# Optimization experiments

Hardware: AMD Instinct MI355X
Metric: run time of the kernel (lower is better)

Reference implementation:

```python
import jax, jax.numpy as jnp
import numpy as np

N, E = 10000, 640000
IN_FT, OUT_FT = 512, 128
NEG_SLOPE = 0.2


def setup_inputs() -> dict:
    key = jax.random.key(0)
    ks = jax.random.split(key, 10)
    seq = jax.random.normal(ks[0], (N, IN_FT), dtype=jnp.float32)
    # edges with no self-loops: dst = (src + offset) % N, offset in [1, N-1]
    src = jax.random.randint(ks[1], (E,), 0, N)
    off = jax.random.randint(ks[2], (E,), 1, N)
    dst = (src + off) % N
    edge_index = jnp.stack([src, dst]).astype(jnp.int64)
    # parameters (xavier-ish scale)
    W_fc = jax.random.normal(ks[3], (OUT_FT, IN_FT), dtype=jnp.float32) * (1.0 / np.sqrt(IN_FT))
    W_gat = jax.random.normal(ks[4], (OUT_FT, OUT_FT), dtype=jnp.float32) * (1.0 / np.sqrt(OUT_FT))
    att_src = jax.random.normal(ks[5], (OUT_FT,), dtype=jnp.float32) * 0.1
    att_dst = jax.random.normal(ks[6], (OUT_FT,), dtype=jnp.float32) * 0.1
    gat_bias = jnp.zeros((OUT_FT,), dtype=jnp.float32)
    bias = jnp.zeros((OUT_FT,), dtype=jnp.float32)
    prelu_a = jnp.asarray(0.25, dtype=jnp.float32)
    return {"seq": seq, "edge_index": edge_index, "W_fc": W_fc, "W_gat": W_gat,
            "att_src": att_src, "att_dst": att_dst, "gat_bias": gat_bias,
            "bias": bias, "prelu_a": prelu_a}


def _gat_forward(seq, src, dst, W_fc, W_gat, att_src, att_dst, gat_bias, bias, prelu_a):
    n = seq.shape[0]
    x = seq @ W_fc.T                      # [N, out_ft] fc (no bias)
    h = x @ W_gat.T                       # GATConv internal linear (no bias)
    a_s = h @ att_src                     # [N] per-node src attention logits
    a_d = h @ att_dst                     # [N]
    e = a_s[src] + a_d[dst]               # [E'] per-edge raw score
    e = jnp.where(e >= 0, e, NEG_SLOPE * e)
    # segment softmax over destination node
    m = jax.ops.segment_max(e, dst, num_segments=n)
    m = jnp.where(jnp.isfinite(m), m, 0.0)
    p = jnp.exp(e - m[dst])
    denom = jax.ops.segment_sum(p, dst, num_segments=n)
    alpha = p / (denom[dst] + 1e-16)
    msgs = alpha[:, None] * h[src]        # [E', out_ft]
    out = jax.ops.segment_sum(msgs, dst, num_segments=n) + gat_bias
    out = out + bias
    return jnp.where(out >= 0, out, prelu_a * out)  # PReLU


def reference(seq, edge_index, W_fc, W_gat, att_src, att_dst, gat_bias, bias, prelu_a):
    n = seq.shape[0]
    loops = jnp.arange(n, dtype=edge_index.dtype)   # add_self_loops
    src = jnp.concatenate([edge_index[0], loops])
    dst = jnp.concatenate([edge_index[1], loops])
    return _gat_forward(seq, src, dst, W_fc, W_gat, att_src, att_dst, gat_bias, bias, prelu_a)
```

## Files before the change

### kernel.cpp

```cpp
#include <hip/hip_runtime.h>
#include <hip/hip_bf16.h>

#define IN_FT 512
#define OUT_FT 128
#define NEG_SLOPE 0.2f
#define SHIFT_C 4.0f
#define CAP8 768
#define NBMAX 1280

typedef __attribute__((ext_vector_type(8))) short short8;
typedef __attribute__((ext_vector_type(4))) short short4v;
typedef __attribute__((ext_vector_type(4))) float float4v;

__device__ inline short f2bf_s(float x) {
    __hip_bfloat16 b = __float2bfloat16(x);
    union { __hip_bfloat16 b; short s; } u;
    u.b = b;
    return u.s;
}
__device__ inline float bf2f(short s) {
    union { float f; unsigned u; } u;
    u.u = ((unsigned)(unsigned short)s) << 16;
    return u.f;
}

__global__ void k_prep(const float* __restrict__ Wg,
                       const float* __restrict__ Wf,
                       short* __restrict__ whf,
                       int* __restrict__ gcur, int nb) {
    if (blockIdx.x >= 256) {
        int i = (blockIdx.x - 256) * 256 + threadIdx.x;
        if (i < nb) gcur[i] = 0;
        return;
    }
    int idx = blockIdx.x * blockDim.x + threadIdx.x;
    int o = idx >> 9;
    int k = idx & 511;
    float s = 0.f;
#pragma unroll 8
    for (int j = 0; j < OUT_FT; ++j)
        s += Wg[o * OUT_FT + j] * Wf[j * IN_FT + k];
    int t = o >> 4, l15 = o & 15;
    int kc = k >> 5, q = (k >> 3) & 3, jj = k & 7;
    whf[(((kc * 8 + t) * 64) + q * 16 + l15) * 8 + jj] = f2bf_s(s);
}

__launch_bounds__(256)
__global__ void k_main(const float* __restrict__ seq,
                       const short8* __restrict__ whf,
                       const float* __restrict__ att_s_v,
                       const float* __restrict__ att_d_v,
                       short* __restrict__ h16,
                       float* __restrict__ a_s,
                       float* __restrict__ a_d,
                       const int* __restrict__ src,
                       const int* __restrict__ dstv,
                       int* __restrict__ gcur,
                       unsigned* __restrict__ bins,
                       int N, int E, int nb, int GB) {
    __shared__ char smem[24576];
    if (blockIdx.x >= GB) {
        int* hist  = (int*)smem;
        int* sbase = hist + NBMAX;
        int* scur  = sbase + NBMAX;
        int e0 = (blockIdx.x - GB) * 2048;
        for (int t = threadIdx.x; t < nb; t += 256) hist[t] = 0;
        __syncthreads();
        int myd[8];
#pragma unroll
        for (int k = 0; k < 8; ++k) {
            int e = e0 + k * 256 + threadIdx.x;
            myd[k] = (e < E) ? dstv[e] : -1;
            if ((unsigned)myd[k] < (unsigned)N) atomicAdd(&hist[myd[k] >> 3], 1);
            else myd[k] = -1;
        }
        __syncthreads();
        for (int t = threadIdx.x; t < nb; t += 256) {
            int c = hist[t];
            sbase[t] = c ? atomicAdd(&gcur[t], c) : 0;
            scur[t] = 0;
        }
        __syncthreads();
#pragma unroll
        for (int k = 0; k < 8; ++k) {
            if (myd[k] >= 0) {
                int e = e0 + k * 256 + threadIdx.x;
                int b = myd[k] >> 3;
                int slot = sbase[b] + atomicAdd(&scur[b], 1);
                if (slot < CAP8) {
                    int s = src[e];
                    if ((unsigned)s >= (unsigned)N) s = 0;
                    bins[(size_t)b * CAP8 + slot] = ((unsigned)s << 3) | (myd[k] & 7);
                }
            }
        }
        return;
    }
    short* As = (short*)smem;
    float4v* red = (float4v*)smem;

    int wave = threadIdx.x >> 6;
    int lane = threadIdx.x & 63;
    int l15 = lane & 15, quad = lane >> 4;
    int rows0 = blockIdx.x * 16;

#pragma unroll
    for (int i = 0; i < 8; ++i) {
        int idx = threadIdx.x + 256 * i;
        int r = idx >> 7, c4 = idx & 127;
        int row = rows0 + r;
        int rowc = row < N ? row : N - 1;
        float4 v = *(const float4*)(seq + (size_t)rowc * IN_FT + c4 * 4);
        short4v b;
        b[0] = f2bf_s(v.x); b[1] = f2bf_s(v.y); b[2] = f2bf_s(v.z); b[3] = f2bf_s(v.w);
        int kc = c4 >> 3, q = (c4 >> 1) & 3, half = c4 & 1;
        *(short4v*)(As + (((kc * 4 + q) * 16 + r) * 8 + half * 4)) = b;
    }
    __syncthreads();

    float4v acc[8];
    for (int t = 0; t < 8; ++t) acc[t] = (float4v){0.f, 0.f, 0.f, 0.f};

#pragma unroll
    for (int kk = 0; kk < 4; ++kk) {
        int kc = wave * 4 + kk;
        short8 a = *(const short8*)(As + ((kc * 4 + quad) * 16 + l15) * 8);
        const short8* bhp = whf + (size_t)kc * 512 + lane;
#pragma unroll
        for (int t = 0; t < 8; ++t) {
            short8 bh = bhp[t * 64];
            acc[t] = __builtin_amdgcn_mfma_f32_16x16x32_bf16(a, bh, acc[t], 0, 0, 0);
        }
    }
    __syncthreads();
    if (wave > 0) {
        float4v* base = red + ((wave - 1) * 8) * 64 + lane;
        for (int t = 0; t < 8; ++t) base[t * 64] = acc[t];
    }
    __syncthreads();
    if (wave != 0) return;
    for (int w2 = 0; w2 < 3; ++w2) {
        const float4v* base = red + (w2 * 8) * 64 + lane;
        for (int t = 0; t < 8; ++t) {
            float4v v = base[t * 64];
            acc[t][0] += v[0]; acc[t][1] += v[1]; acc[t][2] += v[2]; acc[t][3] += v[3];
        }
    }
    int rbase = rows0 + quad * 4;
    for (int r = 0; r < 4; ++r) {
        int rr = rbase + r;
        if (rr < N) {
            short* hr = h16 + (size_t)rr * OUT_FT;
            for (int t = 0; t < 8; ++t) hr[t * 16 + l15] = f2bf_s(acc[t][r]);
        }
    }
    float asv[8], adv[8];
    for (int t = 0; t < 8; ++t) {
        asv[t] = att_s_v[t * 16 + l15];
        adv[t] = att_d_v[t * 16 + l15];
    }
    for (int r = 0; r < 4; ++r) {
        float ps = 0.f, pd = 0.f;
        for (int t = 0; t < 8; ++t) {
            float v = acc[t][r];
            ps += v * asv[t];
            pd += v * adv[t];
        }
        for (int m = 1; m < 16; m <<= 1) {
            ps += __shfl_xor(ps, m);
            pd += __shfl_xor(pd, m);
        }
        int rr = rbase + r;
        if (l15 == 0 && rr < N) { a_s[rr] = ps; a_d[rr] = pd; }
    }
}

__launch_bounds__(256)
__global__ void k_agg(const short* __restrict__ h16, const float* __restrict__ a_s,
                      const float* __restrict__ a_d,
                      const int* __restrict__ gcur, const unsigned* __restrict__ bins,
                      const float* __restrict__ gat_bias,
                      const float* __restrict__ bias,
                      const float* __restrict__ prelu_a,
                      float* __restrict__ out, int N) {
    __shared__ int2  spair[CAP8 + 64];
    __shared__ int   hist[8], base[8], cur8[8];
    __shared__ float ads[8];
    int b = blockIdx.x;
    int d0 = b << 3;
    int nd = N - d0; if (nd > 8) nd = 8;
    int tid = threadIdx.x;

    if (tid < 8) {
        hist[tid] = 0;
        ads[tid] = (tid < nd) ? a_d[d0 + tid] : 0.f;
    }
    __syncthreads();

    int cnt = gcur[b]; if (cnt > CAP8) cnt = CAP8;
    const unsigned* binp = bins + (size_t)b * CAP8;

    for (int c = tid; c < cnt; c += 256) atomicAdd(&hist[binp[c] & 7], 1);
    __syncthreads();
    if (tid == 0) {
        int run = 0;
        for (int i = 0; i < 8; ++i) {
            base[i] = run; cur8[i] = 0;
            run += (hist[i] + 7) & ~7;
        }
    }
    __syncthreads();
    for (int c = tid; c < cnt; c += 256) {
        unsigned pk = binp[c];
        int dl = pk & 7, sv = pk >> 3;
        float ev = a_s[sv] + ads[dl];
        ev = (ev >= 0.f) ? ev : NEG_SLOPE * ev;
        float p = __expf(ev - SHIFT_C);
        int slot = base[dl] + atomicAdd(&cur8[dl], 1);
        int2 sp; sp.x = sv; sp.y = __float_as_int(p);
        spair[slot] = sp;
    }
    if (tid < 64) {
        int dl = tid >> 3, k = tid & 7;
        int n = hist[dl], np = (n + 7) & ~7;
        if (n + k < np) {
            int2 sp; sp.x = d0; sp.y = 0;
            spair[base[dl] + n + k] = sp;
        }
    }
    __syncthreads();

    int w = tid >> 6, L = tid & 63;
    float b0 = gat_bias[2 * L] + bias[2 * L];
    float b1 = gat_bias[2 * L + 1] + bias[2 * L + 1];
    float pa = prelu_a[0];

    int dA = d0 + w, dB = d0 + w + 4;
    int dAc = dA < N ? dA : d0, dBc = dB < N ? dB : d0;
    float eA = a_s[dAc] + ads[w];
    eA = (eA >= 0.f) ? eA : NEG_SLOPE * eA;
    float p0A = __expf(eA - SHIFT_C);
    float eB = a_s[dBc] + ads[(w + 4) & 7];
    eB = (eB >= 0.f) ? eB : NEG_SLOPE * eB;
    float p0B = __expf(eB - SHIFT_C);
    short2 hA = *(const short2*)(h16 + (size_t)dAc * OUT_FT + 2 * L);
    short2 hB = *(const short2*)(h16 + (size_t)dBc * OUT_FT + 2 * L);
    float accA0 = p0A * bf2f(hA.x), accA1 = p0A * bf2f(hA.y), dsA = 0.f;
    float accB0 = p0B * bf2f(hB.x), accB1 = p0B * bf2f(hB.y), dsB = 0.f;

    int nA = (hist[w] + 7) & ~7,     begA = base[w];
    int nB = (hist[w + 4] + 7) & ~7, begB = base[w + 4];
    int nmax = nA > nB ? nA : nB;

    for (int c = 0; c < nmax; c += 8) {
        float ppA[8], ppB[8]; short2 hhA[8], hhB[8];
        bool doA = c < nA, doB = c < nB;
        if (doA) {
#pragma unroll
            for (int j = 0; j < 8; ++j) {
                int2 sp = spair[begA + c + j];
                ppA[j] = __int_as_float(sp.y);
                hhA[j] = *(const short2*)(h16 + (size_t)sp.x * OUT_FT + 2 * L);
            }
        }
        if (doB) {
#pragma unroll
            for (int j = 0; j < 8; ++j) {
                int2 sp = spair[begB + c + j];
                ppB[j] = __int_as_float(sp.y);
                hhB[j] = *(const short2*)(h16 + (size_t)sp.x * OUT_FT + 2 * L);
            }
        }
        if (doA) {
#pragma unroll
            for (int j = 0; j < 8; ++j) {
                dsA += ppA[j];
                accA0 += ppA[j] * bf2f(hhA[j].x);
                accA1 += ppA[j] * bf2f(hhA[j].y);
            }
        }
        if (doB) {
#pragma unroll
            for (int j = 0; j < 8; ++j) {
                dsB += ppB[j];
                accB0 += ppB[j] * bf2f(hhB[j].x);
                accB1 += ppB[j] * bf2f(hhB[j].y);
            }
        }
    }
    if (dA < N) {
        float inv = 1.f / (dsA + p0A + 1e-16f);
        float o0 = accA0 * inv + b0;
        float o1 = accA1 * inv + b1;
        o0 = (o0 >= 0.f) ? o0 : pa * o0;
        o1 = (o1 >= 0.f) ? o1 : pa * o1;
        float2 ov; ov.x = o0; ov.y = o1;
        *(float2*)(out + (size_t)dA * OUT_FT + 2 * L) = ov;
    }
    if (dB < N) {
        float inv = 1.f / (dsB + p0B + 1e-16f);
        float o0 = accB0 * inv + b0;
        float o1 = accB1 * inv + b1;
        o0 = (o0 >= 0.f) ? o0 : pa * o0;
        o1 = (o1 >= 0.f) ? o1 : pa * o1;
        float2 ov; ov.x = o0; ov.y = o1;
        *(float2*)(out + (size_t)dB * OUT_FT + 2 * L) = ov;
    }
}

extern "C" void kernel_launch(void* const* d_in, const int* in_sizes, int n_in,
                              void* d_out, int out_size, void* d_ws, size_t ws_size,
                              hipStream_t stream) {
    const float* seq     = (const float*)d_in[0];
    const int*   ei      = (const int*)d_in[1];
    const float* W_fc    = (const float*)d_in[2];
    const float* W_gat   = (const float*)d_in[3];
    const float* att_src = (const float*)d_in[4];
    const float* att_dst = (const float*)d_in[5];
    const float* gat_b   = (const float*)d_in[6];
    const float* bias    = (const float*)d_in[7];
    const float* prelu_a = (const float*)d_in[8];

    int N = in_sizes[0] / IN_FT;
    int E = in_sizes[1] / 2;
    const int* src = ei;
    const int* dst = ei + E;
    int nb = (N + 7) >> 3;

    char* wsb = (char*)d_ws;
    size_t cur = 0;
    auto alloc = [&](size_t bytes) -> void* {
        void* p = (void*)(wsb + cur);
        cur += (bytes + 255) & ~(size_t)255;
        return p;
    };
    short*    h16  = (short*)alloc((size_t)N * OUT_FT * 2);
    float*    a_s  = (float*)alloc((size_t)N * 4);
    float*    a_d  = (float*)alloc((size_t)N * 4);
    int*      gcur = (int*)alloc((size_t)nb * 4);
    unsigned* bins = (unsigned*)alloc((size_t)nb * CAP8 * 4);
    short*    whf  = (short*)alloc((size_t)OUT_FT * IN_FT * 2);

    int GB = (N + 15) / 16;
    int PB = (E + 2047) / 2048;

    k_prep<<<dim3(256 + (nb + 255) / 256), dim3(256), 0, stream>>>(W_gat, W_fc, whf, gcur, nb);
    k_main<<<dim3(GB + PB), dim3(256), 0, stream>>>(
        seq, (const short8*)whf, att_src, att_dst, h16, a_s, a_d,
        src, dst, gcur, bins, N, E, nb, GB);
    k_agg<<<dim3(nb), dim3(256), 0, stream>>>(
        h16, a_s, a_d, gcur, bins, gat_b, bias, prelu_a, (float*)d_out, N);
}
```

Baseline: 127.7 us.

## Split GEMM output columns across waves with 32-row tiles instead of K-split reduction

The projection GEMM in k_main now processes 32 rows per block, and each wave owns two 16-column output tiles over the full K range. Previously each wave split K and wave 0 reduced partials through shared memory. This removes the LDS reduction pass and lets all four waves write h16 and compute attention partials, which are combined through a small shared buffer. It also halves the GEMM block count, raises LDS use per block, and changes the k_prep unroll factor.

```diff
diff --git a/kernel.cpp b/kernel.cpp
--- a/kernel.cpp
+++ b/kernel.cpp
@@ -37,7 +37,7 @@
     int o = idx >> 9;
     int k = idx & 511;
     float s = 0.f;
-#pragma unroll 8
+#pragma unroll 16
     for (int j = 0; j < OUT_FT; ++j)
         s += Wg[o * OUT_FT + j] * Wf[j * IN_FT + k];
     int t = o >> 4, l15 = o & 15;
@@ -58,7 +58,7 @@
                        int* __restrict__ gcur,
                        unsigned* __restrict__ bins,
                        int N, int E, int nb, int GB) {
-    __shared__ char smem[24576];
+    __shared__ char smem[33792];
     if (blockIdx.x >= GB) {
         int* hist  = (int*)smem;
         int* sbase = hist + NBMAX;
@@ -97,15 +97,14 @@
         return;
     }
     short* As = (short*)smem;
-    float4v* red = (float4v*)smem;
 
     int wave = threadIdx.x >> 6;
     int lane = threadIdx.x & 63;
     int l15 = lane & 15, quad = lane >> 4;
-    int rows0 = blockIdx.x * 16;
-
-#pragma unroll
-    for (int i = 0; i < 8; ++i) {
+    int rows0 = blockIdx.x * 32;
+
+#pragma unroll
+    for (int i = 0; i < 16; ++i) {
         int idx = threadIdx.x + 256 * i;
         int r = idx >> 7, c4 = idx & 127;
         int row = rows0 + r;
@@ -113,65 +112,77 @@
         float4 v = *(const float4*)(seq + (size_t)rowc * IN_FT + c4 * 4);
         short4v b;
         b[0] = f2bf_s(v.x); b[1] = f2bf_s(v.y); b[2] = f2bf_s(v.z); b[3] = f2bf_s(v.w);
+        int rg = r >> 4, r16 = r & 15;
         int kc = c4 >> 3, q = (c4 >> 1) & 3, half = c4 & 1;
-        *(short4v*)(As + (((kc * 4 + q) * 16 + r) * 8 + half * 4)) = b;
-    }
-    __syncthreads();
-
-    float4v acc[8];
-    for (int t = 0; t < 8; ++t) acc[t] = (float4v){0.f, 0.f, 0.f, 0.f};
-
-#pragma unroll
-    for (int kk = 0; kk < 4; ++kk) {
-        int kc = wave * 4 + kk;
-        short8 a = *(const short8*)(As + ((kc * 4 + quad) * 16 + l15) * 8);
-        const short8* bhp = whf + (size_t)kc * 512 + lane;
-#pragma unroll
-        for (int t = 0; t < 8; ++t) {
-            short8 bh = bhp[t * 64];
-            acc[t] = __builtin_amdgcn_mfma_f32_16x16x32_bf16(a, bh, acc[t], 0, 0, 0);
-        }
-    }
-    __syncthreads();
-    if (wave > 0) {
-        float4v* base = red + ((wave - 1) * 8) * 64 + lane;
-        for (int t = 0; t < 8; ++t) base[t * 64] = acc[t];
-    }
-    __syncthreads();
-    if (wave != 0) return;
-    for (int w2 = 0; w2 < 3; ++w2) {
-        const float4v* base = red + (w2 * 8) * 64 + lane;
-        for (int t = 0; t < 8; ++t) {
-            float4v v = base[t * 64];
-            acc[t][0] += v[0]; acc[t][1] += v[1]; acc[t][2] += v[2]; acc[t][3] += v[3];
-        }
-    }
-    int rbase = rows0 + quad * 4;
-    for (int r = 0; r < 4; ++r) {
-        int rr = rbase + r;
+        *(short4v*)(As + rg * 8192 + ((kc * 4 + q) * 16 + r16) * 8 + half * 4) = b;
+    }
+    __syncthreads();
+
+    float4v accs[2][2];
+#pragma unroll
+    for (int rg = 0; rg < 2; ++rg)
+#pragma unroll
+        for (int tt = 0; tt < 2; ++tt) accs[rg][tt] = (float4v){0.f, 0.f, 0.f, 0.f};
+
+    const short8* wp = whf + lane;
+#pragma unroll
+    for (int kc = 0; kc < 16; ++kc) {
+        short8 a0 = *(const short8*)(As + ((kc * 4 + quad) * 16 + l15) * 8);
+        short8 a1 = *(const short8*)(As + 8192 + ((kc * 4 + quad) * 16 + l15) * 8);
+        short8 b0 = wp[(size_t)(kc * 8 + 2 * wave) * 64];
+        short8 b1 = wp[(size_t)(kc * 8 + 2 * wave + 1) * 64];
+        accs[0][0] = __builtin_amdgcn_mfma_f32_16x16x32_bf16(a0, b0, accs[0][0], 0, 0, 0);
+        accs[0][1] = __builtin_amdgcn_mfma_f32_16x16x32_bf16(a0, b1, accs[0][1], 0, 0, 0);
+        accs[1][0] = __builtin_amdgcn_mfma_f32_16x16x32_bf16(a1, b0, accs[1][0], 0, 0, 0);
+        accs[1][1] = __builtin_amdgcn_mfma_f32_16x16x32_bf16(a1, b1, accs[1][1], 0, 0, 0);
+    }
+
+#pragma unroll
+    for (int rg = 0; rg < 2; ++rg)
+#pragma unroll
+        for (int tt = 0; tt < 2; ++tt) {
+            int t = 2 * wave + tt;
+#pragma unroll
+            for (int r = 0; r < 4; ++r) {
+                int rr = rows0 + rg * 16 + quad * 4 + r;
+                if (rr < N)
+                    h16[(size_t)rr * OUT_FT + t * 16 + l15] = f2bf_s(accs[rg][tt][r]);
+            }
+        }
+
+    float asv0 = att_s_v[(2 * wave) * 16 + l15];
+    float asv1 = att_s_v[(2 * wave + 1) * 16 + l15];
+    float adv0 = att_d_v[(2 * wave) * 16 + l15];
+    float adv1 = att_d_v[(2 * wave + 1) * 16 + l15];
+    float* psh = (float*)(smem + 32768);
+    float* pdh = psh + 128;
+#pragma unroll
+    for (int rg = 0; rg < 2; ++rg)
+#pragma unroll
+        for (int r = 0; r < 4; ++r) {
+            float ps = accs[rg][0][r] * asv0 + accs[rg][1][r] * asv1;
+            float pd = accs[rg][0][r] * adv0 + accs[rg][1][r] * adv1;
+#pragma unroll
+            for (int m = 1; m < 16; m <<= 1) {
+                ps += __shfl_xor(ps, m);
+                pd += __shfl_xor(pd, m);
+            }
+            if (l15 == 0) {
+                int row = rg * 16 + quad * 4 + r;
+                psh[wave * 32 + row] = ps;
+                pdh[wave * 32 + row] = pd;
+            }
+        }
+    __syncthreads();
+    if (threadIdx.x < 32) {
+        int rr = rows0 + threadIdx.x;
         if (rr < N) {
-            short* hr = h16 + (size_t)rr * OUT_FT;
-            for (int t = 0; t < 8; ++t) hr[t * 16 + l15] = f2bf_s(acc[t][r]);
-        }
-    }
-    float asv[8], adv[8];
-    for (int t = 0; t < 8; ++t) {
-        asv[t] = att_s_v[t * 16 + l15];
-        adv[t] = att_d_v[t * 16 + l15];
-    }
-    for (int r = 0; r < 4; ++r) {
-        float ps = 0.f, pd = 0.f;
-        for (int t = 0; t < 8; ++t) {
-            float v = acc[t][r];
-            ps += v * asv[t];
-            pd += v * adv[t];
-        }
-        for (int m = 1; m < 16; m <<= 1) {
-            ps += __shfl_xor(ps, m);
-            pd += __shfl_xor(pd, m);
-        }
-        int rr = rbase + r;
-        if (l15 == 0 && rr < N) { a_s[rr] = ps; a_d[rr] = pd; }
+            float s = psh[threadIdx.x] + psh[32 + threadIdx.x] +
+                      psh[64 + threadIdx.x] + psh[96 + threadIdx.x];
+            float d = pdh[threadIdx.x] + pdh[32 + threadIdx.x] +
+                      pdh[64 + threadIdx.x] + pdh[96 + threadIdx.x];
+            a_s[rr] = s; a_d[rr] = d;
+        }
     }
 }
 
@@ -341,7 +352,7 @@
     unsigned* bins = (unsigned*)alloc((size_t)nb * CAP8 * 4);
     short*    whf  = (short*)alloc((size_t)OUT_FT * IN_FT * 2);
 
-    int GB = (N + 15) / 16;
+    int GB = (N + 31) / 32;
     int PB = (E + 2047) / 2048;
 
     k_prep<<<dim3(256 + (nb + 255) / 256), dim3(256), 0, stream>>>(W_gat, W_fc, whf, gcur, nb);
```

Result: no change. 125.7 us (-1.6%).
